# Optimization experiments

Measured on AMD Instinct MI355X. Metric: run time of the kernel, lower is better.

Reference implementation:

```python
import jax, jax.numpy as jnp
import numpy as np

T, N, H, D = 128, 2048, 128, 128  # timesteps, envs, hidden_dim, embedding_dim
EPS = 1e-5


def layer_norm(x, w, b):
    m = x.mean(-1, keepdims=True)
    v = ((x - m) ** 2).mean(-1, keepdims=True)
    return (x - m) * jax.lax.rsqrt(v + EPS) * w + b


def setup_inputs() -> dict:
    key = jax.random.key(0)
    ks = jax.random.split(key, 10)
    s = 0.05
    return {
        "x": jax.random.normal(ks[0], (T * N, D), jnp.float32),
        "hxs": jax.random.normal(ks[1], (N, 1, H), jnp.float32),
        "masks": jax.random.randint(ks[2], (T * N, 1), 0, 2).astype(jnp.float32),
        "ln1_w": jnp.ones((D,), jnp.float32),
        "ln1_b": jnp.zeros((D,), jnp.float32),
        "W1": jax.random.normal(ks[3], (H, D), jnp.float32) * s,
        "b1": jnp.zeros((H,), jnp.float32),
        "W2": jax.random.normal(ks[4], (H, H), jnp.float32) * s,
        "b2": jnp.zeros((H,), jnp.float32),
        "W_ih": jax.random.normal(ks[5], (3 * H, H), jnp.float32) * s,
        "b_ih": jnp.zeros((3 * H,), jnp.float32),
        "W_hh": jax.random.normal(ks[6], (3 * H, H), jnp.float32) * s,
        "b_hh": jnp.zeros((3 * H,), jnp.float32),
        "ln2_w": jnp.ones((H,), jnp.float32),
        "ln2_b": jnp.zeros((H,), jnp.float32),
    }


def reference(x, hxs, masks, ln1_w, ln1_b, W1, b1, W2, b2,
              W_ih, b_ih, W_hh, b_hh, ln2_w, ln2_b):
    # feature norm + two linear layers (no nonlinearity in the original)
    feats = layer_norm(x, ln1_w, ln1_b)            # [T*N, D]
    feats = feats @ W1.T + b1                      # [T*N, H]
    feats = feats @ W2.T + b2                      # [T*N, H]
    feats = feats.reshape(T, N, H)
    m = masks.reshape(T, N)

    # precompute input-side GRU gates once (big GEMM outside the scan)
    gi = feats @ W_ih.T + b_ih                     # [T, N, 3H]

    h0 = hxs[:, 0, :]                              # num_rnn_layers == 1

    def step(h, inp):
        gi_t, m_t = inp
        h = h * m_t[:, None]                       # mask-reset (== segment split)
        gh = h @ W_hh.T + b_hh                     # [N, 3H]
        i_r, i_z, i_n = jnp.split(gi_t, 3, axis=-1)
        h_r, h_z, h_n = jnp.split(gh, 3, axis=-1)
        r = jax.nn.sigmoid(i_r + h_r)
        z = jax.nn.sigmoid(i_z + h_z)
        n = jnp.tanh(i_n + r * h_n)
        h_new = (1.0 - z) * n + z * h
        return h_new, h_new

    hT, outs = jax.lax.scan(step, h0, (gi, m))     # outs: [T, N, H]

    out = layer_norm(outs.reshape(T * N, H), ln2_w, ln2_b)
    return out, hT[:, None, :]
```

## Files before the change

kernel.cpp:

```cpp
#include <hip/hip_runtime.h>

#define Tt 128
#define Nn 2048
#define Hh 128
#define Dd 128
#define NB 8
#define LDA 136
#define LDG 388

#define WC_OFF  0
#define BC_OFF  49152
#define TMP_OFF 49536
#define BT_OFF  65920

typedef __attribute__((ext_vector_type(8))) short v8s;
typedef __attribute__((ext_vector_type(4))) float v4f;
typedef __attribute__((ext_vector_type(2))) float v2f;

__device__ __forceinline__ unsigned short f2bf(float f) {
    unsigned int u = __builtin_bit_cast(unsigned int, f);
    u += 0x7FFFu + ((u >> 16) & 1u);
    return (unsigned short)(u >> 16);
}

__device__ __forceinline__ v4f mfma_bf(v8s a, v8s b, v4f c) {
    return __builtin_amdgcn_mfma_f32_16x16x32_bf16(a, b, c, 0, 0, 0);
}

__device__ __forceinline__ v8s load_wfrag_bf(const float* __restrict__ W, int row, int k0) {
    const v4f* p = (const v4f*)(W + row * 128 + k0);
    v4f a = p[0], b = p[1];
    v8s r;
    r[0] = (short)f2bf(a[0]); r[1] = (short)f2bf(a[1]);
    r[2] = (short)f2bf(a[2]); r[3] = (short)f2bf(a[3]);
    r[4] = (short)f2bf(b[0]); r[5] = (short)f2bf(b[1]);
    r[6] = (short)f2bf(b[2]); r[7] = (short)f2bf(b[3]);
    return r;
}

__device__ __forceinline__ float sigm(float x) { return __frcp_rn(1.f + __expf(-x)); }
__device__ __forceinline__ float tanh_f(float x) {
    return 2.f * __frcp_rn(1.f + __expf(-2.f * x)) - 1.f;
}

#define BARRIER() asm volatile("s_waitcnt lgkmcnt(0)\n\ts_barrier" ::: "memory")

__global__ void prep_tmp(const float* __restrict__ W1, const float* __restrict__ b1,
                         const float* __restrict__ W2, const float* __restrict__ b2,
                         float* __restrict__ ws) {
    float* Tmp = ws + TMP_OFF;
    float* bt  = ws + BT_OFF;
    int j = blockIdx.x, d = threadIdx.x;
    float acc = 0.f;
    for (int k = 0; k < 128; ++k) acc += W2[j * 128 + k] * W1[k * 128 + d];
    Tmp[j * 128 + d] = acc;
    if (d == 0) {
        float s = 0.f;
        for (int k = 0; k < 128; ++k) s += W2[j * 128 + k] * b1[k];
        bt[j] = s + b2[j];
    }
}

__global__ void prep_wc(const float* __restrict__ Wih, const float* __restrict__ bih,
                        float* __restrict__ ws) {
    const float* Tmp = ws + TMP_OFF;
    const float* bt  = ws + BT_OFF;
    float* Wc = ws + WC_OFF;
    float* bc = ws + BC_OFF;
    int r = blockIdx.x, d = threadIdx.x;
    float acc = 0.f;
    for (int j = 0; j < 128; ++j) acc += Wih[r * 128 + j] * Tmp[j * 128 + d];
    Wc[r * 128 + d] = acc;
    if (d == 0) {
        float s = 0.f;
        for (int j = 0; j < 128; ++j) s += Wih[r * 128 + j] * bt[j];
        bc[r] = s + bih[r];
    }
}

__global__ __launch_bounds__(512, 2)
void rppo_scan(const float* __restrict__ x, const float* __restrict__ hxs,
               const float* __restrict__ masks,
               const float* __restrict__ ln1_w, const float* __restrict__ ln1_b,
               const float* __restrict__ Whh, const float* __restrict__ bhh,
               const float* __restrict__ ln2_w, const float* __restrict__ ln2_b,
               const float* __restrict__ ws, float* __restrict__ out)
{
    __shared__ unsigned short fbuf[NB * LDA];
    __shared__ unsigned short hbuf[NB * LDA];
    __shared__ float gibuf[NB * LDG];
    __shared__ float ghbuf[NB * LDG];
    __shared__ float mbuf[Tt * NB];

    const int tid  = threadIdx.x;
    const int wave = tid >> 6;
    const int lane = tid & 63;
    const int l16  = lane & 15;
    const int quad = lane >> 4;
    const int arow = l16 & 7;
    const int wsub = wave & 3;
    const bool isP = (wave < 4);
    const int n0   = blockIdx.x * NB;
    const int r    = wave;
    const int c2   = lane << 1;

    const float* Wc = ws + WC_OFF;
    const float* bc = ws + BC_OFF;

    v8s wreg[6][4];
    float brC[6];
    {
        const float* Wm = isP ? Wc : Whh;
        const float* bm = isP ? bc : bhh;
#pragma unroll
        for (int c = 0; c < 6; ++c) {
            int rowc = (6 * wsub + c) * 16 + l16;
            brC[c] = bm[rowc];
#pragma unroll
            for (int kk = 0; kk < 4; ++kk)
                wreg[c][kk] = load_wfrag_bf(Wm, rowc, kk * 32 + quad * 8);
        }
    }

    for (int idx = tid; idx < Tt * NB; idx += 512) {
        int t = idx >> 3, b = idx & 7;
        mbuf[idx] = masks[t * Nn + n0 + b];
    }

    v2f ln1w2 = *(const v2f*)(ln1_w + c2);
    v2f ln1b2 = *(const v2f*)(ln1_b + c2);
    v2f ln2w2 = *(const v2f*)(ln2_w + c2);
    v2f ln2b2 = *(const v2f*)(ln2_b + c2);

    v2f h = *(const v2f*)(hxs + (size_t)(n0 + r) * Hh + c2);
    float m0 = masks[n0 + r];
    h[0] *= m0; h[1] *= m0;
    *(unsigned int*)(hbuf + r * LDA + c2) =
        (unsigned int)f2bf(h[0]) | ((unsigned int)f2bf(h[1]) << 16);

    v2f xv = *(const v2f*)(x + (size_t)(n0 + r) * Dd + c2);

    __syncthreads();

    for (int i = 0; i <= Tt; ++i) {
        if (i >= 1) {
            const int t = i - 1;
            const float* gb = gibuf + r * LDG + c2;
            const float* hb = ghbuf + r * LDG + c2;
            v2f ir  = *(const v2f*)(gb);
            v2f iz  = *(const v2f*)(gb + 128);
            v2f inn = *(const v2f*)(gb + 256);
            v2f hr  = *(const v2f*)(hb);
            v2f hz  = *(const v2f*)(hb + 128);
            v2f hn  = *(const v2f*)(hb + 256);
            float hn0, hn1;
            {
                float rg = sigm(ir[0] + hr[0]);
                float z  = sigm(iz[0] + hz[0]);
                float n  = tanh_f(inn[0] + rg * hn[0]);
                hn0 = n + z * (h[0] - n);
            }
            {
                float rg = sigm(ir[1] + hr[1]);
                float z  = sigm(iz[1] + hz[1]);
                float n  = tanh_f(inn[1] + rg * hn[1]);
                hn1 = n + z * (h[1] - n);
            }
            float s2 = hn0 + hn1, ss2 = hn0 * hn0 + hn1 * hn1;
#pragma unroll
            for (int m = 1; m < 64; m <<= 1) {
                s2  += __shfl_xor(s2,  m, 64);
                ss2 += __shfl_xor(ss2, m, 64);
            }
            float mu2 = s2 * (1.f / 128.f);
            float rs2 = __frsqrt_rn(ss2 * (1.f / 128.f) - mu2 * mu2 + 1e-5f);
            v2f o;
            o[0] = (hn0 - mu2) * rs2 * ln2w2[0] + ln2b2[0];
            o[1] = (hn1 - mu2) * rs2 * ln2w2[1] + ln2b2[1];
            *(v2f*)(out + ((size_t)t * Nn + n0 + r) * Hh + c2) = o;

            if (t + 1 < Tt) {
                float mt = mbuf[(t + 1) * NB + r];
                h[0] = hn0 * mt; h[1] = hn1 * mt;
                *(unsigned int*)(hbuf + r * LDA + c2) =
                    (unsigned int)f2bf(h[0]) | ((unsigned int)f2bf(h[1]) << 16);
            } else {
                v2f hf; hf[0] = hn0; hf[1] = hn1;
                *(v2f*)(out + (size_t)Tt * Nn * Hh + (size_t)(n0 + r) * Hh + c2) = hf;
            }
        }
        if (i < Tt) {
            float s = xv[0] + xv[1], ss = xv[0] * xv[0] + xv[1] * xv[1];
#pragma unroll
            for (int m = 1; m < 64; m <<= 1) {
                s  += __shfl_xor(s,  m, 64);
                ss += __shfl_xor(ss, m, 64);
            }
            float mu = s * (1.f / 128.f);
            float rs = __frsqrt_rn(ss * (1.f / 128.f) - mu * mu + 1e-5f);
            float f0 = (xv[0] - mu) * rs * ln1w2[0] + ln1b2[0];
            float f1 = (xv[1] - mu) * rs * ln1w2[1] + ln1b2[1];
            *(unsigned int*)(fbuf + r * LDA + c2) =
                (unsigned int)f2bf(f0) | ((unsigned int)f2bf(f1) << 16);
            if (i + 1 < Tt)
                xv = *(const v2f*)(x + ((size_t)(i + 1) * Nn + n0 + r) * Dd + c2);
        }
        BARRIER();

        if (i < Tt) {
            const unsigned short* src = isP ? fbuf : hbuf;
            float* dst = isP ? gibuf : ghbuf;
            v8s af[4];
#pragma unroll
            for (int kk = 0; kk < 4; ++kk)
                af[kk] = *(const v8s*)(src + arow * LDA + kk * 32 + quad * 8);
            v4f acc[6];
#pragma unroll
            for (int c = 0; c < 6; ++c) acc[c] = (v4f){0.f, 0.f, 0.f, 0.f};
#pragma unroll
            for (int c = 0; c < 6; ++c)
#pragma unroll
                for (int kk = 0; kk < 4; ++kk)
                    acc[c] = mfma_bf(af[kk], wreg[c][kk], acc[c]);
#pragma unroll
            for (int c = 0; c < 6; ++c) {
                int col = (6 * wsub + c) * 16 + l16;
#pragma unroll
                for (int rr = 0; rr < 4; ++rr) {
                    int row = quad * 4 + rr;
                    if (row < 8) dst[row * LDG + col] = acc[c][rr] + brC[c];
                }
            }
        }
        BARRIER();
    }
}

extern "C" void kernel_launch(void* const* d_in, const int* in_sizes, int n_in,
                              void* d_out, int out_size, void* d_ws, size_t ws_size,
                              hipStream_t stream) {
    const float* x     = (const float*)d_in[0];
    const float* hxs   = (const float*)d_in[1];
    const float* masks = (const float*)d_in[2];
    const float* ln1w  = (const float*)d_in[3];
    const float* ln1b  = (const float*)d_in[4];
    const float* W1    = (const float*)d_in[5];
    const float* b1    = (const float*)d_in[6];
    const float* W2    = (const float*)d_in[7];
    const float* b2    = (const float*)d_in[8];
    const float* Wih   = (const float*)d_in[9];
    const float* bih   = (const float*)d_in[10];
    const float* Whh   = (const float*)d_in[11];
    const float* bhh   = (const float*)d_in[12];
    const float* ln2w  = (const float*)d_in[13];
    const float* ln2b  = (const float*)d_in[14];
    float* out = (float*)d_out;
    float* ws  = (float*)d_ws;

    hipLaunchKernelGGL(prep_tmp, dim3(128), dim3(128), 0, stream, W1, b1, W2, b2, ws);
    hipLaunchKernelGGL(prep_wc,  dim3(384), dim3(128), 0, stream, Wih, bih, ws);

    hipLaunchKernelGGL(rppo_scan, dim3(Nn / NB), dim3(512), 0, stream,
                       x, hxs, masks, ln1w, ln1b, Whh, bhh, ln2w, ln2b,
                       (const float*)ws, out);
}
```

Measured before the change: 470.7 us.

## Halve envs per block and pack input and hidden rows into one MFMA tile

Each block now handles 4 environments instead of 8, which doubles the grid. The LN1 features and the hidden state share one 8-row bf16 A-tile: rows 0-3 hold the features and rows 4-7 hold the hidden state. Half-waves of 32 lanes each process one row with 4 elements per lane. The aim is more blocks to fill the CUs and fewer wasted MFMA rows per step, at the cost of twice as many blocks each loading the full weight set into registers, and each wave's MFMA now keeping only 4 useful output rows.

```diff
diff --git a/kernel.cpp b/kernel.cpp
--- a/kernel.cpp
+++ b/kernel.cpp
@@ -4,7 +4,7 @@
 #define Nn 2048
 #define Hh 128
 #define Dd 128
-#define NB 8
+#define NB 4
 #define LDA 136
 #define LDG 388
 
@@ -15,7 +15,6 @@
 
 typedef __attribute__((ext_vector_type(8))) short v8s;
 typedef __attribute__((ext_vector_type(4))) float v4f;
-typedef __attribute__((ext_vector_type(2))) float v2f;
 
 __device__ __forceinline__ unsigned short f2bf(float f) {
     unsigned int u = __builtin_bit_cast(unsigned int, f);
@@ -38,10 +37,15 @@
     return r;
 }
 
-__device__ __forceinline__ float sigm(float x) { return __frcp_rn(1.f + __expf(-x)); }
-__device__ __forceinline__ float tanh_f(float x) {
-    return 2.f * __frcp_rn(1.f + __expf(-2.f * x)) - 1.f;
-}
+__device__ __forceinline__ void store_bf4(unsigned short* p, v4f v) {
+    unsigned int lo = ((unsigned int)f2bf(v[1]) << 16) | (unsigned int)f2bf(v[0]);
+    unsigned int hi = ((unsigned int)f2bf(v[3]) << 16) | (unsigned int)f2bf(v[2]);
+    uint2 d; d.x = lo; d.y = hi;
+    *(uint2*)p = d;
+}
+
+__device__ __forceinline__ float sigm(float x)  { return __frcp_rn(1.f + __expf(-x)); }
+__device__ __forceinline__ float tanh_f(float x){ return 2.f * __frcp_rn(1.f + __expf(-2.f * x)) - 1.f; }
 
 #define BARRIER() asm volatile("s_waitcnt lgkmcnt(0)\n\ts_barrier" ::: "memory")
 
@@ -86,8 +90,7 @@
                const float* __restrict__ ln2_w, const float* __restrict__ ln2_b,
                const float* __restrict__ ws, float* __restrict__ out)
 {
-    __shared__ unsigned short fbuf[NB * LDA];
-    __shared__ unsigned short hbuf[NB * LDA];
+    __shared__ unsigned short abuf[8 * LDA];
     __shared__ float gibuf[NB * LDG];
     __shared__ float ghbuf[NB * LDG];
     __shared__ float mbuf[Tt * NB];
@@ -101,8 +104,6 @@
     const int wsub = wave & 3;
     const bool isP = (wave < 4);
     const int n0   = blockIdx.x * NB;
-    const int r    = wave;
-    const int c2   = lane << 1;
 
     const float* Wc = ws + WC_OFF;
     const float* bc = ws + BC_OFF;
@@ -122,98 +123,100 @@
         }
     }
 
-    for (int idx = tid; idx < Tt * NB; idx += 512) {
-        int t = idx >> 3, b = idx & 7;
-        mbuf[idx] = masks[t * Nn + n0 + b];
-    }
-
-    v2f ln1w2 = *(const v2f*)(ln1_w + c2);
-    v2f ln1b2 = *(const v2f*)(ln1_b + c2);
-    v2f ln2w2 = *(const v2f*)(ln2_w + c2);
-    v2f ln2b2 = *(const v2f*)(ln2_b + c2);
-
-    v2f h = *(const v2f*)(hxs + (size_t)(n0 + r) * Hh + c2);
-    float m0 = masks[n0 + r];
-    h[0] *= m0; h[1] *= m0;
-    *(unsigned int*)(hbuf + r * LDA + c2) =
-        (unsigned int)f2bf(h[0]) | ((unsigned int)f2bf(h[1]) << 16);
-
-    v2f xv = *(const v2f*)(x + (size_t)(n0 + r) * Dd + c2);
-
+    {
+        int t = tid >> 2, b = tid & 3;
+        mbuf[tid] = masks[t * Nn + n0 + b];
+    }
+
+    const int g      = tid >> 5;
+    const bool doLN  = (g < 4);
+    const bool doTl  = (g >= 8) && (g < 12);
+    const int brow   = doLN ? g : (g - 8);
+    const int col4   = (lane & 31) << 2;
+
+    v4f lnw = {0.f,0.f,0.f,0.f}, lnb = {0.f,0.f,0.f,0.f}, hx = {0.f,0.f,0.f,0.f};
+    if (doLN) {
+        lnw = *(const v4f*)(ln1_w + col4);
+        lnb = *(const v4f*)(ln1_b + col4);
+        hx  = *(const v4f*)(x + (size_t)(n0 + brow) * Dd + col4);
+    } else if (doTl) {
+        lnw = *(const v4f*)(ln2_w + col4);
+        lnb = *(const v4f*)(ln2_b + col4);
+        hx  = *(const v4f*)(hxs + (size_t)(n0 + brow) * Hh + col4);
+        float m0 = masks[n0 + brow];
+#pragma unroll
+        for (int e = 0; e < 4; ++e) hx[e] *= m0;
+        store_bf4(abuf + (4 + brow) * LDA + col4, hx);
+    }
     __syncthreads();
 
     for (int i = 0; i <= Tt; ++i) {
-        if (i >= 1) {
+        if (doLN) {
+            if (i < Tt) {
+                float s  = hx[0] + hx[1] + hx[2] + hx[3];
+                float ss = hx[0]*hx[0] + hx[1]*hx[1] + hx[2]*hx[2] + hx[3]*hx[3];
+#pragma unroll
+                for (int m = 1; m < 32; m <<= 1) {
+                    s  += __shfl_xor(s,  m, 64);
+                    ss += __shfl_xor(ss, m, 64);
+                }
+                float mu = s * (1.f / 128.f);
+                float rs = __frsqrt_rn(ss * (1.f / 128.f) - mu * mu + 1e-5f);
+                v4f f;
+#pragma unroll
+                for (int e = 0; e < 4; ++e) f[e] = (hx[e] - mu) * rs * lnw[e] + lnb[e];
+                store_bf4(abuf + brow * LDA + col4, f);
+                if (i + 1 < Tt)
+                    hx = *(const v4f*)(x + ((size_t)(i + 1) * Nn + n0 + brow) * Dd + col4);
+            }
+        } else if (doTl && i >= 1) {
             const int t = i - 1;
-            const float* gb = gibuf + r * LDG + c2;
-            const float* hb = ghbuf + r * LDG + c2;
-            v2f ir  = *(const v2f*)(gb);
-            v2f iz  = *(const v2f*)(gb + 128);
-            v2f inn = *(const v2f*)(gb + 256);
-            v2f hr  = *(const v2f*)(hb);
-            v2f hz  = *(const v2f*)(hb + 128);
-            v2f hn  = *(const v2f*)(hb + 256);
-            float hn0, hn1;
-            {
-                float rg = sigm(ir[0] + hr[0]);
-                float z  = sigm(iz[0] + hz[0]);
-                float n  = tanh_f(inn[0] + rg * hn[0]);
-                hn0 = n + z * (h[0] - n);
-            }
-            {
-                float rg = sigm(ir[1] + hr[1]);
-                float z  = sigm(iz[1] + hz[1]);
-                float n  = tanh_f(inn[1] + rg * hn[1]);
-                hn1 = n + z * (h[1] - n);
-            }
-            float s2 = hn0 + hn1, ss2 = hn0 * hn0 + hn1 * hn1;
-#pragma unroll
-            for (int m = 1; m < 64; m <<= 1) {
+            const float* gb = gibuf + brow * LDG + col4;
+            const float* hb = ghbuf + brow * LDG + col4;
+            v4f ir  = *(const v4f*)(gb);
+            v4f iz  = *(const v4f*)(gb + 128);
+            v4f inn = *(const v4f*)(gb + 256);
+            v4f hr  = *(const v4f*)(hb);
+            v4f hz  = *(const v4f*)(hb + 128);
+            v4f hn  = *(const v4f*)(hb + 256);
+            v4f hnew;
+#pragma unroll
+            for (int e = 0; e < 4; ++e) {
+                float rg = sigm(ir[e] + hr[e]);
+                float z  = sigm(iz[e] + hz[e]);
+                float n  = tanh_f(inn[e] + rg * hn[e]);
+                hnew[e] = n + z * (hx[e] - n);
+            }
+            float s2  = hnew[0] + hnew[1] + hnew[2] + hnew[3];
+            float ss2 = hnew[0]*hnew[0] + hnew[1]*hnew[1] + hnew[2]*hnew[2] + hnew[3]*hnew[3];
+#pragma unroll
+            for (int m = 1; m < 32; m <<= 1) {
                 s2  += __shfl_xor(s2,  m, 64);
                 ss2 += __shfl_xor(ss2, m, 64);
             }
             float mu2 = s2 * (1.f / 128.f);
             float rs2 = __frsqrt_rn(ss2 * (1.f / 128.f) - mu2 * mu2 + 1e-5f);
-            v2f o;
-            o[0] = (hn0 - mu2) * rs2 * ln2w2[0] + ln2b2[0];
-            o[1] = (hn1 - mu2) * rs2 * ln2w2[1] + ln2b2[1];
-            *(v2f*)(out + ((size_t)t * Nn + n0 + r) * Hh + c2) = o;
+            v4f o;
+#pragma unroll
+            for (int e = 0; e < 4; ++e) o[e] = (hnew[e] - mu2) * rs2 * lnw[e] + lnb[e];
+            *(v4f*)(out + ((size_t)t * Nn + n0 + brow) * Hh + col4) = o;
 
             if (t + 1 < Tt) {
-                float mt = mbuf[(t + 1) * NB + r];
-                h[0] = hn0 * mt; h[1] = hn1 * mt;
-                *(unsigned int*)(hbuf + r * LDA + c2) =
-                    (unsigned int)f2bf(h[0]) | ((unsigned int)f2bf(h[1]) << 16);
+                float mt = mbuf[(t + 1) * NB + brow];
+#pragma unroll
+                for (int e = 0; e < 4; ++e) hx[e] = hnew[e] * mt;
+                store_bf4(abuf + (4 + brow) * LDA + col4, hx);
             } else {
-                v2f hf; hf[0] = hn0; hf[1] = hn1;
-                *(v2f*)(out + (size_t)Tt * Nn * Hh + (size_t)(n0 + r) * Hh + c2) = hf;
-            }
-        }
-        if (i < Tt) {
-            float s = xv[0] + xv[1], ss = xv[0] * xv[0] + xv[1] * xv[1];
-#pragma unroll
-            for (int m = 1; m < 64; m <<= 1) {
-                s  += __shfl_xor(s,  m, 64);
-                ss += __shfl_xor(ss, m, 64);
-            }
-            float mu = s * (1.f / 128.f);
-            float rs = __frsqrt_rn(ss * (1.f / 128.f) - mu * mu + 1e-5f);
-            float f0 = (xv[0] - mu) * rs * ln1w2[0] + ln1b2[0];
-            float f1 = (xv[1] - mu) * rs * ln1w2[1] + ln1b2[1];
-            *(unsigned int*)(fbuf + r * LDA + c2) =
-                (unsigned int)f2bf(f0) | ((unsigned int)f2bf(f1) << 16);
-            if (i + 1 < Tt)
-                xv = *(const v2f*)(x + ((size_t)(i + 1) * Nn + n0 + r) * Dd + c2);
+                *(v4f*)(out + (size_t)Tt * Nn * Hh + (size_t)(n0 + brow) * Hh + col4) = hnew;
+            }
         }
         BARRIER();
 
         if (i < Tt) {
-            const unsigned short* src = isP ? fbuf : hbuf;
-            float* dst = isP ? gibuf : ghbuf;
             v8s af[4];
 #pragma unroll
             for (int kk = 0; kk < 4; ++kk)
-                af[kk] = *(const v8s*)(src + arow * LDA + kk * 32 + quad * 8);
+                af[kk] = *(const v8s*)(abuf + arow * LDA + kk * 32 + quad * 8);
             v4f acc[6];
 #pragma unroll
             for (int c = 0; c < 6; ++c) acc[c] = (v4f){0.f, 0.f, 0.f, 0.f};
@@ -222,13 +225,25 @@
 #pragma unroll
                 for (int kk = 0; kk < 4; ++kk)
                     acc[c] = mfma_bf(af[kk], wreg[c][kk], acc[c]);
-#pragma unroll
-            for (int c = 0; c < 6; ++c) {
-                int col = (6 * wsub + c) * 16 + l16;
-#pragma unroll
-                for (int rr = 0; rr < 4; ++rr) {
-                    int row = quad * 4 + rr;
-                    if (row < 8) dst[row * LDG + col] = acc[c][rr] + brC[c];
+            if (isP) {
+                if (quad == 0) {
+#pragma unroll
+                    for (int c = 0; c < 6; ++c) {
+                        int col = (6 * wsub + c) * 16 + l16;
+#pragma unroll
+                        for (int rr = 0; rr < 4; ++rr)
+                            gibuf[rr * LDG + col] = acc[c][rr] + brC[c];
+                    }
+                }
+            } else {
+                if (quad == 1) {
+#pragma unroll
+                    for (int c = 0; c < 6; ++c) {
+                        int col = (6 * wsub + c) * 16 + l16;
+#pragma unroll
+                        for (int rr = 0; rr < 4; ++rr)
+                            ghbuf[rr * LDG + col] = acc[c][rr] + brC[c];
+                    }
                 }
             }
         }
```

Measured after the change: 656.9 us. 1.4x slower.
